# Kernel optimization log

Hardware: AMD Instinct MI355X
Metric: run time of the kernel (lower is better)

The kernel has to match this reference:

```python
import jax, jax.numpy as jnp
import numpy as np

MASK_LOGIT_CONST = 1000000000.0
LN_EPS = 1e-12


def setup_inputs() -> dict:
    key = jax.random.key(0)
    k_in, k_w = jax.random.split(key)
    B, S, H = 8, 2048, 1024
    inputs = jax.random.normal(k_in, (B, S, H), dtype=jnp.float32)
    masks = jnp.ones((B, S, S), dtype=jnp.float32)
    w_match = jax.random.normal(k_w, (2 * H, H), dtype=jnp.float32) * (1.0 / np.sqrt(2 * H))
    b_match = jnp.zeros((H,), dtype=jnp.float32)
    ln_gamma = jnp.ones((H,), dtype=jnp.float32)
    ln_beta = jnp.zeros((H,), dtype=jnp.float32)
    return {"inputs": inputs, "masks": masks, "w_match": w_match,
            "b_match": b_match, "ln_gamma": ln_gamma, "ln_beta": ln_beta}


def reference(inputs, masks, w_match, b_match, ln_gamma, ln_beta):
    H = inputs.shape[-1]
    scale = 1.0 / jnp.sqrt(jnp.asarray(H, dtype=inputs.dtype))
    # self-attention scores [B,S,S] (dropout disabled -> query=key=inputs)
    scores = jnp.einsum('bsh,bth->bst', inputs, inputs) * scale
    # logits_mask: scores*mask + (-C)*(1-mask)
    scores = scores * masks - MASK_LOGIT_CONST * (1.0 - masks)
    probs = jax.nn.softmax(scores, axis=-1)
    context = jnp.einsum('bst,bth->bsh', probs, inputs)
    cat = jnp.concatenate([inputs, context], axis=-1)  # [B,S,2H]
    matching = jnp.einsum('bsk,kh->bsh', cat, w_match) + b_match
    # layernorm over last dim
    mu = jnp.mean(matching, axis=-1, keepdims=True)
    var = jnp.mean((matching - mu) ** 2, axis=-1, keepdims=True)
    normed = (matching - mu) * jax.lax.rsqrt(var + LN_EPS)
    return normed * ln_gamma + ln_beta
```

## Files before the change

kernel.cpp:

```cpp
#include <hip/hip_runtime.h>
#include <hip/hip_bf16.h>
#include <hip/hip_fp8.h>


typedef unsigned short ushort_t;
typedef __attribute__((ext_vector_type(8))) short short8;
typedef __attribute__((ext_vector_type(4))) float float4v;
typedef __attribute__((ext_vector_type(2))) long long2v;

__device__ inline float b2f(unsigned int u) {
    union { unsigned int i; float f; } v; v.i = u << 16; return v.f;
}
__device__ inline ushort_t f2b(float f) {
    __hip_bfloat16 h = __float2bfloat16(f);
    return __builtin_bit_cast(ushort_t, h);
}
__device__ inline unsigned char f2e4(float f) {
    return __hip_fp8_e4m3(f).__x;
}

__device__ inline void gload_lds16(const void* g, void* lds) {
    __builtin_amdgcn_global_load_lds(
        (const __attribute__((address_space(1))) unsigned int*)g,
        (__attribute__((address_space(3))) unsigned int*)lds, 16, 0, 0);
}

template<int EPI>
__global__ __launch_bounds__(512, 2)
void gemm_bt(const ushort_t* __restrict__ A, const ushort_t* __restrict__ A2, int kSplit,
             const ushort_t* __restrict__ B,
             int M, int N, int K, int lda, int ldb, int ldc,
             long aBS, long bBS, long cBS,
             const float* __restrict__ rowsum,
             const float* __restrict__ bias,
             ushort_t* __restrict__ outb)
{
    __shared__ __align__(16) ushort_t smem[4 * 16384];

    const int tid = threadIdx.x;
    const int z = blockIdx.z;
    A  += (size_t)z * aBS;
    A2 += (size_t)z * aBS;
    B  += (size_t)z * bBS;
    if (EPI == 2) rowsum += (size_t)z * M;
    outb += (size_t)z * cBS;

    const int bm = blockIdx.x * 256;
    const int bn = blockIdx.y * 256;
    const int w = tid >> 6, lane = tid & 63;
    const int wm = (w >> 2) * 128, wn = (w & 3) * 64;
    const int q = lane >> 4, l15 = lane & 15;
    const int srow = lane >> 2;
    const int schunk = ((lane & 3) ^ ((lane >> 3) & 3)) * 8;

    float4v acc[8][4];
#pragma unroll
    for (int i = 0; i < 8; i++)
#pragma unroll
        for (int j = 0; j < 4; j++) acc[i][j] = (float4v){0.f, 0.f, 0.f, 0.f};

    const int NT = K >> 5;

#define STAGE(T) do {                                                               \
        const int k0_ = (T) * 32;                                                   \
        const ushort_t* aS_ = A; int ka_ = k0_;                                     \
        if (k0_ >= kSplit) { aS_ = A2; ka_ = k0_ - kSplit; }                        \
        ushort_t* buf_ = &smem[((T) & 3) * 16384];                                  \
        gload_lds16(aS_ + (size_t)(bm + w * 16       + srow) * lda + ka_ + schunk,  \
                    buf_ + w * 512);                                                \
        gload_lds16(aS_ + (size_t)(bm + (w + 8) * 16 + srow) * lda + ka_ + schunk,  \
                    buf_ + (w + 8) * 512);                                          \
        gload_lds16(B   + (size_t)(bn + w * 16       + srow) * ldb + k0_ + schunk,  \
                    buf_ + 8192 + w * 512);                                         \
        gload_lds16(B   + (size_t)(bn + (w + 8) * 16 + srow) * ldb + k0_ + schunk,  \
                    buf_ + 8192 + (w + 8) * 512);                                   \
    } while (0)

    STAGE(0); STAGE(1); STAGE(2);

    for (int T = 0; T < NT; ++T) {
        if (T + 2 < NT)      asm volatile("s_waitcnt vmcnt(8)\n\ts_barrier" ::: "memory");
        else if (T + 1 < NT) asm volatile("s_waitcnt vmcnt(4)\n\ts_barrier" ::: "memory");
        else                 asm volatile("s_waitcnt vmcnt(0)\n\ts_barrier" ::: "memory");

        if (T + 3 < NT) STAGE(T + 3);

        const ushort_t* bufA = &smem[(T & 3) * 16384];
        const ushort_t* bufB = bufA + 8192;
        short8 af[8], bf[4];
#pragma unroll
        for (int mi = 0; mi < 8; mi++) {
            const int r = wm + mi * 16 + l15;
            af[mi] = *(const short8*)(&bufA[r * 32 + ((q ^ ((r >> 1) & 3)) << 3)]);
        }
#pragma unroll
        for (int ni = 0; ni < 4; ni++) {
            const int r = wn + ni * 16 + l15;
            bf[ni] = *(const short8*)(&bufB[r * 32 + ((q ^ ((r >> 1) & 3)) << 3)]);
        }
        __builtin_amdgcn_s_setprio(1);
#pragma unroll
        for (int mi = 0; mi < 8; mi++)
#pragma unroll
            for (int ni = 0; ni < 4; ni++)
                acc[mi][ni] = __builtin_amdgcn_mfma_f32_16x16x32_bf16(
                    af[mi], bf[ni], acc[mi][ni], 0, 0, 0);
        __builtin_amdgcn_s_setprio(0);
    }
#undef STAGE

#pragma unroll
    for (int mi = 0; mi < 8; mi++) {
#pragma unroll
        for (int r = 0; r < 4; r++) {
            const int row = bm + wm + mi * 16 + q * 4 + r;
            const size_t ro = (size_t)row * ldc;
            float rsinv = 1.f;
            if (EPI == 2) rsinv = 1.0f / rowsum[row];
#pragma unroll
            for (int ni = 0; ni < 4; ni++) {
                const int col = bn + wn + ni * 16 + l15;
                float v = acc[mi][ni][r];
                if (EPI == 2) outb[ro + col] = f2b(v * rsinv);
                else          outb[ro + col] = f2b(v + bias[col]);
            }
        }
    }
}

__global__ __launch_bounds__(512, 2)
void gemm1_fp8(const unsigned char* __restrict__ X8,
               const float* __restrict__ mask,
               float* __restrict__ rowsum,
               ushort_t* __restrict__ E)
{
    __shared__ __align__(16) unsigned char smem[4 * 32768];

    const int tid = threadIdx.x;
    const int z = blockIdx.z;
    const unsigned char* Xz = X8 + (size_t)z * 2048 * 1024;
    const float* mz = mask + (size_t)z * 2048 * 2048;
    float* rsz = rowsum + (size_t)z * 2048;
    ushort_t* Ez = E + (size_t)z * 2048 * 2048;

    const int bm = blockIdx.x * 256;
    const int bn = blockIdx.y * 256;
    const int w = tid >> 6, lane = tid & 63;
    const int wm = (w >> 2) * 128, wn = (w & 3) * 64;
    const int q = lane >> 4, l15 = lane & 15;
    const int srow = lane >> 2;
    const int schunk = ((lane & 3) ^ ((lane >> 3) & 3)) * 16;

    float4v acc[8][4];
#pragma unroll
    for (int i = 0; i < 8; i++)
#pragma unroll
        for (int j = 0; j < 4; j++) acc[i][j] = (float4v){0.f, 0.f, 0.f, 0.f};

#define STAGE1(T) do {                                                                        \
        const int k0_ = (T) * 64;                                                             \
        unsigned char* buf_ = &smem[((T) & 3) * 32768];                                       \
        gload_lds16(Xz + (size_t)(bm + w * 16        + srow) * 1024 + k0_ + schunk,           \
                    buf_ + w * 1024);                                                         \
        gload_lds16(Xz + (size_t)(bm + 128 + w * 16  + srow) * 1024 + k0_ + schunk,           \
                    buf_ + 8192 + w * 1024);                                                  \
        gload_lds16(Xz + (size_t)(bn + w * 16        + srow) * 1024 + k0_ + schunk,           \
                    buf_ + 16384 + w * 1024);                                                 \
        gload_lds16(Xz + (size_t)(bn + 128 + w * 16  + srow) * 1024 + k0_ + schunk,           \
                    buf_ + 16384 + 8192 + w * 1024);                                          \
    } while (0)

    STAGE1(0); STAGE1(1); STAGE1(2);

    for (int T = 0; T < 16; ++T) {
        if (T < 14)      asm volatile("s_waitcnt vmcnt(8)\n\ts_barrier" ::: "memory");
        else if (T < 15) asm volatile("s_waitcnt vmcnt(4)\n\ts_barrier" ::: "memory");
        else             asm volatile("s_waitcnt vmcnt(0)\n\ts_barrier" ::: "memory");

        if (T + 3 < 16) STAGE1(T + 3);

        const unsigned char* bufA = &smem[(T & 3) * 32768];
        const unsigned char* bufB = bufA + 16384;
        long2v af[8], bf[4];
#pragma unroll
        for (int mi = 0; mi < 8; mi++) {
            const int r = wm + mi * 16 + l15;
            af[mi] = *(const long2v*)(&bufA[r * 64 + ((q ^ ((r >> 1) & 3)) << 4)]);
        }
#pragma unroll
        for (int ni = 0; ni < 4; ni++) {
            const int r = wn + ni * 16 + l15;
            bf[ni] = *(const long2v*)(&bufB[r * 64 + ((q ^ ((r >> 1) & 3)) << 4)]);
        }
        __builtin_amdgcn_s_setprio(1);
#pragma unroll
        for (int s = 0; s < 2; s++)
#pragma unroll
            for (int mi = 0; mi < 8; mi++)
#pragma unroll
                for (int ni = 0; ni < 4; ni++)
                    acc[mi][ni] = __builtin_amdgcn_mfma_f32_16x16x32_fp8_fp8(
                        af[mi][s], bf[ni][s], acc[mi][ni], 0, 0, 0);
        __builtin_amdgcn_s_setprio(0);
    }
#undef STAGE1

    const float scale = 0.03125f;
#pragma unroll
    for (int mi = 0; mi < 8; mi++) {
#pragma unroll
        for (int r = 0; r < 4; r++) {
            const int row = bm + wm + mi * 16 + q * 4 + r;
            const size_t ro = (size_t)row * 2048;
            float s = 0.f;
#pragma unroll
            for (int ni = 0; ni < 4; ni++) {
                const int col = bn + wn + ni * 16 + l15;
                const float m = mz[ro + col];
                float v = __expf(acc[mi][ni][r] * scale * m - 1e9f * (1.0f - m));
                s += v;
                Ez[ro + col] = f2b(v);
            }
            s += __shfl_xor(s, 8);
            s += __shfl_xor(s, 4);
            s += __shfl_xor(s, 2);
            s += __shfl_xor(s, 1);
            if (l15 == 0) atomicAdd(&rsz[row], s);
        }
    }
}

__global__ __launch_bounds__(256)
void conv_trans(const float* __restrict__ in, ushort_t* __restrict__ outT,
                ushort_t* __restrict__ outS, unsigned char* __restrict__ outQ,
                int R, int C)
{
    __shared__ float tile[64][65];
    const int tx = threadIdx.x & 15, ty = threadIdx.x >> 4;
    const size_t zoff = (size_t)blockIdx.z * R * C;
    const int r0 = blockIdx.y * 64, c0 = blockIdx.x * 64;
#pragma unroll
    for (int j = 0; j < 4; j++) {
        const int r = ty + j * 16;
        const float4 v = *(const float4*)(in + zoff + (size_t)(r0 + r) * C + c0 + tx * 4);
        tile[r][tx * 4 + 0] = v.x;
        tile[r][tx * 4 + 1] = v.y;
        tile[r][tx * 4 + 2] = v.z;
        tile[r][tx * 4 + 3] = v.w;
        if (outS) {
            ushort4 o;
            o.x = f2b(v.x); o.y = f2b(v.y); o.z = f2b(v.z); o.w = f2b(v.w);
            *(ushort4*)(outS + zoff + (size_t)(r0 + r) * C + c0 + tx * 4) = o;
            uchar4 p;
            p.x = f2e4(v.x); p.y = f2e4(v.y); p.z = f2e4(v.z); p.w = f2e4(v.w);
            *(uchar4*)(outQ + zoff + (size_t)(r0 + r) * C + c0 + tx * 4) = p;
        }
    }
    __syncthreads();
    ushort_t* tp = outT + zoff;
#pragma unroll
    for (int j = 0; j < 4; j++) {
        const int cc = ty + j * 16;
        ushort4 o;
        o.x = f2b(tile[tx * 4 + 0][cc]);
        o.y = f2b(tile[tx * 4 + 1][cc]);
        o.z = f2b(tile[tx * 4 + 2][cc]);
        o.w = f2b(tile[tx * 4 + 3][cc]);
        *(ushort4*)(tp + (size_t)(c0 + cc) * R + r0 + tx * 4) = o;
    }
}

__global__ __launch_bounds__(256)
void ln_k(const ushort_t* __restrict__ Mt, const float* __restrict__ gamma,
          const float* __restrict__ beta, float* __restrict__ out)
{
    const size_t row = blockIdx.x;
    const int tid = threadIdx.x;
    const ushort4 u = *(const ushort4*)(Mt + row * 1024 + tid * 4);
    float x0 = b2f(u.x), x1 = b2f(u.y), x2 = b2f(u.z), x3 = b2f(u.w);
    float s  = x0 + x1 + x2 + x3;
    float s2 = x0 * x0 + x1 * x1 + x2 * x2 + x3 * x3;
#pragma unroll
    for (int off = 32; off > 0; off >>= 1) {
        s  += __shfl_down(s, off);
        s2 += __shfl_down(s2, off);
    }
    __shared__ float red[8];
    const int wave = tid >> 6, lane = tid & 63;
    if (lane == 0) { red[wave] = s; red[4 + wave] = s2; }
    __syncthreads();
    s  = red[0] + red[1] + red[2] + red[3];
    s2 = red[4] + red[5] + red[6] + red[7];
    const float mu  = s * (1.0f / 1024.0f);
    const float var = s2 * (1.0f / 1024.0f) - mu * mu;
    const float rinv = rsqrtf(var + 1e-12f);
    const float4 g = *(const float4*)(gamma + tid * 4);
    const float4 b = *(const float4*)(beta + tid * 4);
    float4 o;
    o.x = (x0 - mu) * rinv * g.x + b.x;
    o.y = (x1 - mu) * rinv * g.y + b.y;
    o.z = (x2 - mu) * rinv * g.z + b.z;
    o.w = (x3 - mu) * rinv * g.w + b.w;
    *(float4*)(out + row * 1024 + tid * 4) = o;
}

extern "C" void kernel_launch(void* const* d_in, const int* in_sizes, int n_in,
                              void* d_out, int out_size, void* d_ws, size_t ws_size,
                              hipStream_t stream)
{
    const float* X     = (const float*)d_in[0];
    const float* masks = (const float*)d_in[1];
    const float* Wm    = (const float*)d_in[2];
    const float* bias  = (const float*)d_in[3];
    const float* gamma = (const float*)d_in[4];
    const float* beta  = (const float*)d_in[5];
    float* out = (float*)d_out;
    char* ws = (char*)d_ws;

    const int B = 8, S = 2048, H = 1024;

    ushort_t* Xb  = (ushort_t*)(ws);
    ushort_t* XT  = (ushort_t*)(ws + 33554432);
    ushort_t* WT  = (ushort_t*)(ws + 67108864);
    ushort_t* E   = (ushort_t*)(ws + 71303168);
    float*    rs  = (float*)   (ws + 138412032);
    ushort_t* CTX = (ushort_t*)(ws + 138477568);
    unsigned char* X8 = (unsigned char*)CTX;
    ushort_t* matching = E;

    conv_trans<<<dim3(16, 32, 8), 256, 0, stream>>>(X, XT, Xb, X8, S, H);
    conv_trans<<<dim3(16, 32, 1), 256, 0, stream>>>(Wm, WT, nullptr, nullptr, 2 * H, H);
    hipMemsetAsync(rs, 0, (size_t)B * S * sizeof(float), stream);

    gemm1_fp8<<<dim3(8, 8, 8), 512, 0, stream>>>(X8, masks, rs, E);

    gemm_bt<2><<<dim3(8, 4, 8), 512, 0, stream>>>(
        E, E, 1 << 30, XT,
        S, H, S, S, S, H,
        (long)S * S, (long)H * S, (long)S * H,
        rs, nullptr, CTX);

    gemm_bt<3><<<dim3(64, 4, 1), 512, 0, stream>>>(
        Xb, CTX, H, WT,
        B * S, H, 2 * H, H, 2 * H, H,
        0, 0, 0,
        nullptr, bias, matching);

    ln_k<<<B * S, 256, 0, stream>>>(matching, gamma, beta, out);
}
```

Before: 502.4 us.

## Software-pipeline LDS fragment loads with MFMA via register double buffering

Both GEMM main loops now load the next k-step's operand fragments from LDS into a second register set while the MFMAs for the current step run, unrolled by two to alternate the buffers. The fp8 kernel also halves its k-tile from 64 to 32, cutting LDS per block from 128KB to 64KB, and changes the load swizzle and staging layout to match. The aim is to hide LDS read latency behind matrix math and to allow more resident blocks. In exchange it raises register pressure and doubles the number of barriers per k in the fp8 kernel.

```diff
diff --git a/kernel.cpp b/kernel.cpp
--- a/kernel.cpp
+++ b/kernel.cpp
@@ -6,7 +6,6 @@
 typedef unsigned short ushort_t;
 typedef __attribute__((ext_vector_type(8))) short short8;
 typedef __attribute__((ext_vector_type(4))) float float4v;
-typedef __attribute__((ext_vector_type(2))) long long2v;
 
 __device__ inline float b2f(unsigned int u) {
     union { unsigned int i; float f; } v; v.i = u << 16; return v.f;
@@ -76,38 +75,66 @@
                     buf_ + 8192 + (w + 8) * 512);                                   \
     } while (0)
 
+#define LOAD_AF(dst, bufA_) do {                                                    \
+        _Pragma("unroll")                                                           \
+        for (int mi_ = 0; mi_ < 8; mi_++) {                                         \
+            const int r_ = wm + mi_ * 16 + l15;                                     \
+            dst[mi_] = *(const short8*)(&(bufA_)[r_ * 32 + ((q ^ ((r_ >> 1) & 3)) << 3)]); \
+        } } while (0)
+
+#define LOAD_BF(dst, bufB_) do {                                                    \
+        _Pragma("unroll")                                                           \
+        for (int ni_ = 0; ni_ < 4; ni_++) {                                         \
+            const int r_ = wn + ni_ * 16 + l15;                                     \
+            dst[ni_] = *(const short8*)(&(bufB_)[r_ * 32 + ((q ^ ((r_ >> 1) & 3)) << 3)]); \
+        } } while (0)
+
+#define MFMA_BT(afx) do {                                                           \
+        __builtin_amdgcn_s_setprio(1);                                              \
+        _Pragma("unroll")                                                           \
+        for (int mi_ = 0; mi_ < 8; mi_++)                                           \
+            _Pragma("unroll")                                                       \
+            for (int ni_ = 0; ni_ < 4; ni_++)                                       \
+                acc[mi_][ni_] = __builtin_amdgcn_mfma_f32_16x16x32_bf16(            \
+                    afx[mi_], bfS[ni_], acc[mi_][ni_], 0, 0, 0);                    \
+        __builtin_amdgcn_s_setprio(0); } while (0)
+
+    short8 afA[8], afB[8], bfS[4];
+
     STAGE(0); STAGE(1); STAGE(2);
-
-    for (int T = 0; T < NT; ++T) {
-        if (T + 2 < NT)      asm volatile("s_waitcnt vmcnt(8)\n\ts_barrier" ::: "memory");
-        else if (T + 1 < NT) asm volatile("s_waitcnt vmcnt(4)\n\ts_barrier" ::: "memory");
-        else                 asm volatile("s_waitcnt vmcnt(0)\n\ts_barrier" ::: "memory");
-
-        if (T + 3 < NT) STAGE(T + 3);
-
-        const ushort_t* bufA = &smem[(T & 3) * 16384];
-        const ushort_t* bufB = bufA + 8192;
-        short8 af[8], bf[4];
-#pragma unroll
-        for (int mi = 0; mi < 8; mi++) {
-            const int r = wm + mi * 16 + l15;
-            af[mi] = *(const short8*)(&bufA[r * 32 + ((q ^ ((r >> 1) & 3)) << 3)]);
-        }
-#pragma unroll
-        for (int ni = 0; ni < 4; ni++) {
-            const int r = wn + ni * 16 + l15;
-            bf[ni] = *(const short8*)(&bufB[r * 32 + ((q ^ ((r >> 1) & 3)) << 3)]);
-        }
-        __builtin_amdgcn_s_setprio(1);
-#pragma unroll
-        for (int mi = 0; mi < 8; mi++)
-#pragma unroll
-            for (int ni = 0; ni < 4; ni++)
-                acc[mi][ni] = __builtin_amdgcn_mfma_f32_16x16x32_bf16(
-                    af[mi], bf[ni], acc[mi][ni], 0, 0, 0);
-        __builtin_amdgcn_s_setprio(0);
+    asm volatile("s_waitcnt vmcnt(8)\n\ts_barrier" ::: "memory");
+    LOAD_AF(afA, (&smem[0]));
+    LOAD_BF(bfS, (&smem[8192]));
+
+    for (int T = 0; T < NT; T += 2) {
+        {
+            if (T + 2 < NT) asm volatile("s_waitcnt vmcnt(4)\n\ts_barrier" ::: "memory");
+            else            asm volatile("s_waitcnt vmcnt(0)\n\ts_barrier" ::: "memory");
+            if (T + 3 < NT) STAGE(T + 3);
+            const ushort_t* nb = &smem[((T + 1) & 3) * 16384];
+            LOAD_AF(afB, nb);
+            MFMA_BT(afA);
+            LOAD_BF(bfS, (nb + 8192));
+        }
+        {
+            const int U = T + 1;
+            if (U + 1 < NT) {
+                if (U + 2 < NT) asm volatile("s_waitcnt vmcnt(4)\n\ts_barrier" ::: "memory");
+                else            asm volatile("s_waitcnt vmcnt(0)\n\ts_barrier" ::: "memory");
+                if (U + 3 < NT) STAGE(U + 3);
+                const ushort_t* nb = &smem[((U + 1) & 3) * 16384];
+                LOAD_AF(afA, nb);
+                MFMA_BT(afB);
+                LOAD_BF(bfS, (nb + 8192));
+            } else {
+                MFMA_BT(afB);
+            }
+        }
     }
 #undef STAGE
+#undef LOAD_AF
+#undef LOAD_BF
+#undef MFMA_BT
 
 #pragma unroll
     for (int mi = 0; mi < 8; mi++) {
@@ -134,7 +161,7 @@
                float* __restrict__ rowsum,
                ushort_t* __restrict__ E)
 {
-    __shared__ __align__(16) unsigned char smem[4 * 32768];
+    __shared__ __align__(16) unsigned char smem[4 * 16384];
 
     const int tid = threadIdx.x;
     const int z = blockIdx.z;
@@ -148,8 +175,8 @@
     const int w = tid >> 6, lane = tid & 63;
     const int wm = (w >> 2) * 128, wn = (w & 3) * 64;
     const int q = lane >> 4, l15 = lane & 15;
-    const int srow = lane >> 2;
-    const int schunk = ((lane & 3) ^ ((lane >> 3) & 3)) * 16;
+    const int srow = lane >> 1;
+    const int sch = ((lane & 1) ^ ((lane >> 3) & 1)) * 16;
 
     float4v acc[8][4];
 #pragma unroll
@@ -157,53 +184,67 @@
 #pragma unroll
         for (int j = 0; j < 4; j++) acc[i][j] = (float4v){0.f, 0.f, 0.f, 0.f};
 
-#define STAGE1(T) do {                                                                        \
-        const int k0_ = (T) * 64;                                                             \
-        unsigned char* buf_ = &smem[((T) & 3) * 32768];                                       \
-        gload_lds16(Xz + (size_t)(bm + w * 16        + srow) * 1024 + k0_ + schunk,           \
-                    buf_ + w * 1024);                                                         \
-        gload_lds16(Xz + (size_t)(bm + 128 + w * 16  + srow) * 1024 + k0_ + schunk,           \
-                    buf_ + 8192 + w * 1024);                                                  \
-        gload_lds16(Xz + (size_t)(bn + w * 16        + srow) * 1024 + k0_ + schunk,           \
-                    buf_ + 16384 + w * 1024);                                                 \
-        gload_lds16(Xz + (size_t)(bn + 128 + w * 16  + srow) * 1024 + k0_ + schunk,           \
-                    buf_ + 16384 + 8192 + w * 1024);                                          \
+#define STAGE1(T) do {                                                              \
+        const int k0_ = (T) * 32;                                                   \
+        unsigned char* buf_ = &smem[((T) & 3) * 16384];                             \
+        gload_lds16(Xz + (size_t)(bm + w * 32 + srow) * 1024 + k0_ + sch,           \
+                    buf_ + w * 1024);                                               \
+        gload_lds16(Xz + (size_t)(bn + w * 32 + srow) * 1024 + k0_ + sch,           \
+                    buf_ + 8192 + w * 1024);                                        \
     } while (0)
 
+#define LOAD1(afx, bfx, buf_) do {                                                  \
+        _Pragma("unroll")                                                           \
+        for (int mi_ = 0; mi_ < 8; mi_++) {                                         \
+            const int r_ = wm + mi_ * 16 + l15;                                     \
+            afx[mi_] = *(const long*)(&(buf_)[r_ * 32 + ((q ^ (((r_ >> 2) & 1) << 1)) << 3)]); \
+        }                                                                           \
+        _Pragma("unroll")                                                           \
+        for (int ni_ = 0; ni_ < 4; ni_++) {                                         \
+            const int r_ = wn + ni_ * 16 + l15;                                     \
+            bfx[ni_] = *(const long*)(&(buf_)[8192 + r_ * 32 + ((q ^ (((r_ >> 2) & 1) << 1)) << 3)]); \
+        } } while (0)
+
+#define MFMA1(afx, bfx) do {                                                        \
+        __builtin_amdgcn_s_setprio(1);                                              \
+        _Pragma("unroll")                                                           \
+        for (int mi_ = 0; mi_ < 8; mi_++)                                           \
+            _Pragma("unroll")                                                       \
+            for (int ni_ = 0; ni_ < 4; ni_++)                                       \
+                acc[mi_][ni_] = __builtin_amdgcn_mfma_f32_16x16x32_fp8_fp8(         \
+                    afx[mi_], bfx[ni_], acc[mi_][ni_], 0, 0, 0);                    \
+        __builtin_amdgcn_s_setprio(0); } while (0)
+
+    long afA[8], bfA[4], afB[8], bfB[4];
+
     STAGE1(0); STAGE1(1); STAGE1(2);
-
-    for (int T = 0; T < 16; ++T) {
-        if (T < 14)      asm volatile("s_waitcnt vmcnt(8)\n\ts_barrier" ::: "memory");
-        else if (T < 15) asm volatile("s_waitcnt vmcnt(4)\n\ts_barrier" ::: "memory");
-        else             asm volatile("s_waitcnt vmcnt(0)\n\ts_barrier" ::: "memory");
-
-        if (T + 3 < 16) STAGE1(T + 3);
-
-        const unsigned char* bufA = &smem[(T & 3) * 32768];
-        const unsigned char* bufB = bufA + 16384;
-        long2v af[8], bf[4];
-#pragma unroll
-        for (int mi = 0; mi < 8; mi++) {
-            const int r = wm + mi * 16 + l15;
-            af[mi] = *(const long2v*)(&bufA[r * 64 + ((q ^ ((r >> 1) & 3)) << 4)]);
-        }
-#pragma unroll
-        for (int ni = 0; ni < 4; ni++) {
-            const int r = wn + ni * 16 + l15;
-            bf[ni] = *(const long2v*)(&bufB[r * 64 + ((q ^ ((r >> 1) & 3)) << 4)]);
-        }
-        __builtin_amdgcn_s_setprio(1);
-#pragma unroll
-        for (int s = 0; s < 2; s++)
-#pragma unroll
-            for (int mi = 0; mi < 8; mi++)
-#pragma unroll
-                for (int ni = 0; ni < 4; ni++)
-                    acc[mi][ni] = __builtin_amdgcn_mfma_f32_16x16x32_fp8_fp8(
-                        af[mi][s], bf[ni][s], acc[mi][ni], 0, 0, 0);
-        __builtin_amdgcn_s_setprio(0);
+    asm volatile("s_waitcnt vmcnt(4)\n\ts_barrier" ::: "memory");
+    LOAD1(afA, bfA, (&smem[0]));
+
+    for (int T = 0; T < 32; T += 2) {
+        {
+            if (T + 2 < 32) asm volatile("s_waitcnt vmcnt(2)\n\ts_barrier" ::: "memory");
+            else            asm volatile("s_waitcnt vmcnt(0)\n\ts_barrier" ::: "memory");
+            if (T + 3 < 32) STAGE1(T + 3);
+            LOAD1(afB, bfB, (&smem[((T + 1) & 3) * 16384]));
+            MFMA1(afA, bfA);
+        }
+        {
+            const int U = T + 1;
+            if (U + 1 < 32) {
+                if (U + 2 < 32) asm volatile("s_waitcnt vmcnt(2)\n\ts_barrier" ::: "memory");
+                else            asm volatile("s_waitcnt vmcnt(0)\n\ts_barrier" ::: "memory");
+                if (U + 3 < 32) STAGE1(U + 3);
+                LOAD1(afA, bfA, (&smem[((U + 1) & 3) * 16384]));
+                MFMA1(afB, bfB);
+            } else {
+                MFMA1(afB, bfB);
+            }
+        }
     }
 #undef STAGE1
+#undef LOAD1
+#undef MFMA1
 
     const float scale = 0.03125f;
 #pragma unroll
```

Result: slower. 1.484 ms (+195.4%).

## Interleave global-to-LDS loads with MFMA phases in both GEMM main loops

Applied to the files above, without the earlier changes.

Restructures the bf16 GEMM and fp8 score GEMM main loops into sub-phases (2 for bf16, 4 for fp8). Each phase loads part of the fragments from LDS, issues one slice of the next stage's global-to-LDS copies, then runs a quarter or half of the MFMAs, separated by barriers. The aim is to spread memory issue across compute and cut fragment register pressure by holding fewer A/B fragments live. In exchange it adds more barriers per k-step, and the extra synchronisation could stall waves.

```diff
diff --git a/kernel.cpp b/kernel.cpp
--- a/kernel.cpp
+++ b/kernel.cpp
@@ -61,35 +61,32 @@
 
     const int NT = K >> 5;
 
-#define STAGE(T) do {                                                               \
-        const int k0_ = (T) * 32;                                                   \
-        const ushort_t* aS_ = A; int ka_ = k0_;                                     \
-        if (k0_ >= kSplit) { aS_ = A2; ka_ = k0_ - kSplit; }                        \
-        ushort_t* buf_ = &smem[((T) & 3) * 16384];                                  \
-        gload_lds16(aS_ + (size_t)(bm + w * 16       + srow) * lda + ka_ + schunk,  \
-                    buf_ + w * 512);                                                \
-        gload_lds16(aS_ + (size_t)(bm + (w + 8) * 16 + srow) * lda + ka_ + schunk,  \
-                    buf_ + (w + 8) * 512);                                          \
-        gload_lds16(B   + (size_t)(bn + w * 16       + srow) * ldb + k0_ + schunk,  \
-                    buf_ + 8192 + w * 512);                                         \
-        gload_lds16(B   + (size_t)(bn + (w + 8) * 16 + srow) * ldb + k0_ + schunk,  \
-                    buf_ + 8192 + (w + 8) * 512);                                   \
-    } while (0)
-
-    STAGE(0); STAGE(1); STAGE(2);
-
-    for (int T = 0; T < NT; ++T) {
-        if (T + 2 < NT)      asm volatile("s_waitcnt vmcnt(8)\n\ts_barrier" ::: "memory");
-        else if (T + 1 < NT) asm volatile("s_waitcnt vmcnt(4)\n\ts_barrier" ::: "memory");
-        else                 asm volatile("s_waitcnt vmcnt(0)\n\ts_barrier" ::: "memory");
-
-        if (T + 3 < NT) STAGE(T + 3);
-
-        const ushort_t* bufA = &smem[(T & 3) * 16384];
+    auto stageA = [&](int T) {
+        const int k0 = T * 32;
+        const ushort_t* aS = A; int ka = k0;
+        if (k0 >= kSplit) { aS = A2; ka = k0 - kSplit; }
+        ushort_t* buf = &smem[(T & 3) * 16384];
+        gload_lds16(aS + (size_t)(bm + w * 16       + srow) * lda + ka + schunk, buf + w * 512);
+        gload_lds16(aS + (size_t)(bm + (w + 8) * 16 + srow) * lda + ka + schunk, buf + (w + 8) * 512);
+    };
+    auto stageB = [&](int T) {
+        const int k0 = T * 32;
+        ushort_t* buf = &smem[(T & 3) * 16384] + 8192;
+        gload_lds16(B + (size_t)(bn + w * 16       + srow) * ldb + k0 + schunk, buf + w * 512);
+        gload_lds16(B + (size_t)(bn + (w + 8) * 16 + srow) * ldb + k0 + schunk, buf + (w + 8) * 512);
+    };
+
+    stageA(0); stageB(0); stageA(1); stageB(1); stageA(2); stageB(2);
+    asm volatile("s_waitcnt vmcnt(8)" ::: "memory");
+    __builtin_amdgcn_s_barrier();
+
+    short8 af[4], bf[4];
+    for (int t = 0; t < NT; ++t) {
+        const ushort_t* bufA = &smem[(t & 3) * 16384];
         const ushort_t* bufB = bufA + 8192;
-        short8 af[8], bf[4];
-#pragma unroll
-        for (int mi = 0; mi < 8; mi++) {
+
+#pragma unroll
+        for (int mi = 0; mi < 4; mi++) {
             const int r = wm + mi * 16 + l15;
             af[mi] = *(const short8*)(&bufA[r * 32 + ((q ^ ((r >> 1) & 3)) << 3)]);
         }
@@ -98,16 +95,38 @@
             const int r = wn + ni * 16 + l15;
             bf[ni] = *(const short8*)(&bufB[r * 32 + ((q ^ ((r >> 1) & 3)) << 3)]);
         }
-        __builtin_amdgcn_s_setprio(1);
-#pragma unroll
-        for (int mi = 0; mi < 8; mi++)
+        if (t + 3 < NT) stageA(t + 3);
+        __builtin_amdgcn_s_barrier();
+        __builtin_amdgcn_s_setprio(1);
+#pragma unroll
+        for (int mi = 0; mi < 4; mi++)
 #pragma unroll
             for (int ni = 0; ni < 4; ni++)
                 acc[mi][ni] = __builtin_amdgcn_mfma_f32_16x16x32_bf16(
                     af[mi], bf[ni], acc[mi][ni], 0, 0, 0);
         __builtin_amdgcn_s_setprio(0);
-    }
-#undef STAGE
+        __builtin_amdgcn_s_barrier();
+
+#pragma unroll
+        for (int mi = 0; mi < 4; mi++) {
+            const int r = wm + 64 + mi * 16 + l15;
+            af[mi] = *(const short8*)(&bufA[r * 32 + ((q ^ ((r >> 1) & 3)) << 3)]);
+        }
+        if (t + 3 < NT) stageB(t + 3);
+        __builtin_amdgcn_s_barrier();
+        __builtin_amdgcn_s_setprio(1);
+#pragma unroll
+        for (int mi = 0; mi < 4; mi++)
+#pragma unroll
+            for (int ni = 0; ni < 4; ni++)
+                acc[4 + mi][ni] = __builtin_amdgcn_mfma_f32_16x16x32_bf16(
+                    af[mi], bf[ni], acc[4 + mi][ni], 0, 0, 0);
+        __builtin_amdgcn_s_setprio(0);
+        if (t + 3 < NT)      asm volatile("s_waitcnt vmcnt(8)" ::: "memory");
+        else if (t + 2 < NT) asm volatile("s_waitcnt vmcnt(4)" ::: "memory");
+        else if (t + 1 < NT) asm volatile("s_waitcnt vmcnt(0)" ::: "memory");
+        __builtin_amdgcn_s_barrier();
+    }
 
 #pragma unroll
     for (int mi = 0; mi < 8; mi++) {
@@ -157,53 +176,107 @@
 #pragma unroll
         for (int j = 0; j < 4; j++) acc[i][j] = (float4v){0.f, 0.f, 0.f, 0.f};
 
-#define STAGE1(T) do {                                                                        \
-        const int k0_ = (T) * 64;                                                             \
-        unsigned char* buf_ = &smem[((T) & 3) * 32768];                                       \
-        gload_lds16(Xz + (size_t)(bm + w * 16        + srow) * 1024 + k0_ + schunk,           \
-                    buf_ + w * 1024);                                                         \
-        gload_lds16(Xz + (size_t)(bm + 128 + w * 16  + srow) * 1024 + k0_ + schunk,           \
-                    buf_ + 8192 + w * 1024);                                                  \
-        gload_lds16(Xz + (size_t)(bn + w * 16        + srow) * 1024 + k0_ + schunk,           \
-                    buf_ + 16384 + w * 1024);                                                 \
-        gload_lds16(Xz + (size_t)(bn + 128 + w * 16  + srow) * 1024 + k0_ + schunk,           \
-                    buf_ + 16384 + 8192 + w * 1024);                                          \
-    } while (0)
-
-    STAGE1(0); STAGE1(1); STAGE1(2);
-
-    for (int T = 0; T < 16; ++T) {
-        if (T < 14)      asm volatile("s_waitcnt vmcnt(8)\n\ts_barrier" ::: "memory");
-        else if (T < 15) asm volatile("s_waitcnt vmcnt(4)\n\ts_barrier" ::: "memory");
-        else             asm volatile("s_waitcnt vmcnt(0)\n\ts_barrier" ::: "memory");
-
-        if (T + 3 < 16) STAGE1(T + 3);
-
-        const unsigned char* bufA = &smem[(T & 3) * 32768];
+    auto stage = [&](int T, int piece) {
+        const int k0 = T * 64;
+        unsigned char* buf = &smem[(T & 3) * 32768] + ((piece & 2) ? 16384 : 0);
+        const int base = (piece & 2) ? bn : bm;
+        const int rowoff = (piece & 1) * 128;
+        gload_lds16(Xz + (size_t)(base + rowoff + w * 16 + srow) * 1024 + k0 + schunk,
+                    buf + rowoff * 64 + w * 1024);
+    };
+
+#pragma unroll
+    for (int T = 0; T < 3; T++) {
+        stage(T, 0); stage(T, 1); stage(T, 2); stage(T, 3);
+    }
+    asm volatile("s_waitcnt vmcnt(8)" ::: "memory");
+    __builtin_amdgcn_s_barrier();
+
+    long2v af[4], bfA[2], bfB[2];
+    const int NT = 16;
+    for (int t = 0; t < NT; ++t) {
+        const unsigned char* bufA = &smem[(t & 3) * 32768];
         const unsigned char* bufB = bufA + 16384;
-        long2v af[8], bf[4];
-#pragma unroll
-        for (int mi = 0; mi < 8; mi++) {
+
+#pragma unroll
+        for (int mi = 0; mi < 4; mi++) {
             const int r = wm + mi * 16 + l15;
             af[mi] = *(const long2v*)(&bufA[r * 64 + ((q ^ ((r >> 1) & 3)) << 4)]);
         }
 #pragma unroll
-        for (int ni = 0; ni < 4; ni++) {
+        for (int ni = 0; ni < 2; ni++) {
             const int r = wn + ni * 16 + l15;
-            bf[ni] = *(const long2v*)(&bufB[r * 64 + ((q ^ ((r >> 1) & 3)) << 4)]);
-        }
+            bfA[ni] = *(const long2v*)(&bufB[r * 64 + ((q ^ ((r >> 1) & 3)) << 4)]);
+        }
+        if (t + 3 < NT) stage(t + 3, 0);
+        __builtin_amdgcn_s_barrier();
         __builtin_amdgcn_s_setprio(1);
 #pragma unroll
         for (int s = 0; s < 2; s++)
 #pragma unroll
-            for (int mi = 0; mi < 8; mi++)
-#pragma unroll
-                for (int ni = 0; ni < 4; ni++)
+            for (int mi = 0; mi < 4; mi++)
+#pragma unroll
+                for (int ni = 0; ni < 2; ni++)
                     acc[mi][ni] = __builtin_amdgcn_mfma_f32_16x16x32_fp8_fp8(
-                        af[mi][s], bf[ni][s], acc[mi][ni], 0, 0, 0);
-        __builtin_amdgcn_s_setprio(0);
-    }
-#undef STAGE1
+                        af[mi][s], bfA[ni][s], acc[mi][ni], 0, 0, 0);
+        __builtin_amdgcn_s_setprio(0);
+        __builtin_amdgcn_s_barrier();
+
+#pragma unroll
+        for (int ni = 0; ni < 2; ni++) {
+            const int r = wn + 32 + ni * 16 + l15;
+            bfB[ni] = *(const long2v*)(&bufB[r * 64 + ((q ^ ((r >> 1) & 3)) << 4)]);
+        }
+        if (t + 3 < NT) stage(t + 3, 1);
+        __builtin_amdgcn_s_barrier();
+        __builtin_amdgcn_s_setprio(1);
+#pragma unroll
+        for (int s = 0; s < 2; s++)
+#pragma unroll
+            for (int mi = 0; mi < 4; mi++)
+#pragma unroll
+                for (int ni = 0; ni < 2; ni++)
+                    acc[mi][2 + ni] = __builtin_amdgcn_mfma_f32_16x16x32_fp8_fp8(
+                        af[mi][s], bfB[ni][s], acc[mi][2 + ni], 0, 0, 0);
+        __builtin_amdgcn_s_setprio(0);
+        __builtin_amdgcn_s_barrier();
+
+#pragma unroll
+        for (int mi = 0; mi < 4; mi++) {
+            const int r = wm + 64 + mi * 16 + l15;
+            af[mi] = *(const long2v*)(&bufA[r * 64 + ((q ^ ((r >> 1) & 3)) << 4)]);
+        }
+        if (t + 3 < NT) stage(t + 3, 2);
+        __builtin_amdgcn_s_barrier();
+        __builtin_amdgcn_s_setprio(1);
+#pragma unroll
+        for (int s = 0; s < 2; s++)
+#pragma unroll
+            for (int mi = 0; mi < 4; mi++)
+#pragma unroll
+                for (int ni = 0; ni < 2; ni++)
+                    acc[4 + mi][2 + ni] = __builtin_amdgcn_mfma_f32_16x16x32_fp8_fp8(
+                        af[mi][s], bfB[ni][s], acc[4 + mi][2 + ni], 0, 0, 0);
+        __builtin_amdgcn_s_setprio(0);
+        __builtin_amdgcn_s_barrier();
+
+        if (t + 3 < NT) stage(t + 3, 3);
+        __builtin_amdgcn_s_barrier();
+        __builtin_amdgcn_s_setprio(1);
+#pragma unroll
+        for (int s = 0; s < 2; s++)
+#pragma unroll
+            for (int mi = 0; mi < 4; mi++)
+#pragma unroll
+                for (int ni = 0; ni < 2; ni++)
+                    acc[4 + mi][ni] = __builtin_amdgcn_mfma_f32_16x16x32_fp8_fp8(
+                        af[mi][s], bfA[ni][s], acc[4 + mi][ni], 0, 0, 0);
+        __builtin_amdgcn_s_setprio(0);
+        if (t + 3 < NT)      asm volatile("s_waitcnt vmcnt(8)" ::: "memory");
+        else if (t + 2 < NT) asm volatile("s_waitcnt vmcnt(4)" ::: "memory");
+        else if (t + 1 < NT) asm volatile("s_waitcnt vmcnt(0)" ::: "memory");
+        __builtin_amdgcn_s_barrier();
+    }
 
     const float scale = 0.03125f;
 #pragma unroll
```

New measurement: 497.4 us. About the same (-1.0%).
